# Performance work log

Hardware: AMD Instinct MI355X
Metric: run time of the kernel (lower is better)

## Reference

```python
import jax, jax.numpy as jnp
import numpy as np

NUM_HEADS = 4
NUM_GROUPS = 8
EPS = 1e-5


def setup_inputs() -> dict:
    key = jax.random.key(0)
    ks = jax.random.split(key, 5)
    B, C, H, W = 16, 512, 32, 32
    s = 1.0 / np.sqrt(C)
    return {
        "x": jax.random.normal(ks[0], (B, C, H, W), dtype=jnp.float32),
        "norm_w": jnp.ones((C,), jnp.float32),
        "norm_b": jnp.zeros((C,), jnp.float32),
        "q_w": jax.random.normal(ks[1], (C, C), jnp.float32) * s,
        "q_b": jnp.zeros((C,), jnp.float32),
        "k_w": jax.random.normal(ks[2], (C, C), jnp.float32) * s,
        "k_b": jnp.zeros((C,), jnp.float32),
        "v_w": jax.random.normal(ks[3], (C, C), jnp.float32) * s,
        "v_b": jnp.zeros((C,), jnp.float32),
        "p_w": jax.random.normal(ks[4], (C, C), jnp.float32) * s,
        "p_b": jnp.zeros((C,), jnp.float32),
    }


def _group_norm(x, w, b):
    # x: (B, C, N) -> GroupNorm over (C//G, N) per group
    B, C, N = x.shape
    g = x.reshape(B, NUM_GROUPS, C // NUM_GROUPS, N)
    mean = g.mean(axis=(2, 3), keepdims=True)
    var = g.var(axis=(2, 3), keepdims=True)
    g = (g - mean) * jax.lax.rsqrt(var + EPS)
    x = g.reshape(B, C, N)
    return x * w[None, :, None] + b[None, :, None]


def reference(x, norm_w, norm_b, q_w, q_b, k_w, k_b, v_w, v_b, p_w, p_b):
    B, C, H, W = x.shape
    N = H * W
    Ch = C // NUM_HEADS  # channels per head
    h = _group_norm(x.reshape(B, C, N), norm_w, norm_b)
    # 1x1 Conv1d == channel matmul: (o c, b c n -> b o n)
    q = jnp.einsum('oc,bcn->bon', q_w, h) + q_b[None, :, None]
    k = jnp.einsum('oc,bcn->bon', k_w, h) + k_b[None, :, None]
    v = jnp.einsum('oc,bcn->bon', v_w, h) + v_b[None, :, None]
    q = q.reshape(B, NUM_HEADS, Ch, N)
    k = k.reshape(B, NUM_HEADS, Ch, N)
    v = v.reshape(B, NUM_HEADS, Ch, N)
    attn = jnp.einsum('bhcn,bhcm->bhnm', q, k) * (1.0 / np.sqrt(Ch))
    attn = jax.nn.softmax(attn, axis=-1)
    out = jnp.einsum('bhnm,bhcm->bhcn', attn, v).reshape(B, C, N)
    out = jnp.einsum('oc,bcn->bon', p_w, out) + p_b[None, :, None]
    return x + out.reshape(B, C, H, W)
```

## Files before the change

kernel.cpp:

```cpp
#include <hip/hip_runtime.h>
#include <hip/hip_bf16.h>
#include <math.h>

#define B_    16
#define C_    512
#define N_    1024
#define G_    8
#define HEADS 4
#define CH    128
#define EPS   1e-5f

typedef __attribute__((ext_vector_type(8))) short short8;
typedef __attribute__((ext_vector_type(4))) float f32x4;
typedef __attribute__((ext_vector_type(16))) float f32x16;
typedef __attribute__((ext_vector_type(4))) int i32x4;

__device__ __forceinline__ unsigned short f2bf(float f) {
  union { float f; unsigned int i; } x; x.f = f;
  unsigned int r = x.i + 0x7FFFu + ((x.i >> 16) & 1u);
  return (unsigned short)(r >> 16);
}

__global__ __launch_bounds__(256) void gn_part(const float* __restrict__ x,
                                               float2* __restrict__ psum) {
  int blk = blockIdx.x;
  const float4* p4 = (const float4*)(x + (size_t)blk * 16384);
  float s = 0.f, ss = 0.f;
  for (int i = threadIdx.x; i < 4096; i += 256) {
    float4 v = p4[i];
    s  += v.x + v.y + v.z + v.w;
    ss += v.x * v.x + v.y * v.y + v.z * v.z + v.w * v.w;
  }
  for (int o = 32; o; o >>= 1) { s += __shfl_down(s, o); ss += __shfl_down(ss, o); }
  __shared__ float ls[4], lss[4];
  int wid = threadIdx.x >> 6, lane = threadIdx.x & 63;
  if (lane == 0) { ls[wid] = s; lss[wid] = ss; }
  __syncthreads();
  if (threadIdx.x == 0) {
    float2 r;
    r.x = (ls[0] + ls[1]) + (ls[2] + ls[3]);
    r.y = (lss[0] + lss[1]) + (lss[2] + lss[3]);
    psum[blk] = r;
  }
}

__global__ __launch_bounds__(256) void conv_w(const float* __restrict__ q, const float* __restrict__ k,
                                              const float* __restrict__ v, const float* __restrict__ p,
                                              const float* __restrict__ qb, const float* __restrict__ kb,
                                              unsigned short* __restrict__ dst,
                                              float* __restrict__ qkb) {
  const int n = C_ * C_;
  int i = blockIdx.x * 256 + threadIdx.x;
  if (i < n) {
    dst[i]         = f2bf(q[i]);
    dst[n + i]     = f2bf(k[i]);
    dst[2 * n + i] = f2bf(v[i]);
    dst[3 * n + i] = f2bf(p[i]);
  }
  if (i < 1024) qkb[i] = (i < 512) ? qb[i] : kb[i - 512];
}

__global__ __launch_bounds__(256) void gn_apply(const float* __restrict__ x,
                                                const float2* __restrict__ psum,
                                                const float* __restrict__ gw,
                                                const float* __restrict__ gb,
                                                unsigned short* __restrict__ hT) {
  __shared__ float T[64][65];
  int b = blockIdx.z, c0 = blockIdx.y * 64, n0 = blockIdx.x * 64;
  int bg = b * G_ + (c0 >> 6);
  float2 p0 = psum[bg * 4 + 0], p1 = psum[bg * 4 + 1];
  float2 p2 = psum[bg * 4 + 2], p3 = psum[bg * 4 + 3];
  const float inv = 1.f / ((C_ / G_) * N_);
  float mean = ((p0.x + p1.x) + (p2.x + p3.x)) * inv;
  float var  = ((p0.y + p1.y) + (p2.y + p3.y)) * inv - mean * mean;
  float rstd = rsqrtf(var + EPS);
  int t = threadIdx.x;
  for (int it = 0; it < 4; it++) {
    int L = it * 256 + t;
    int cc = L >> 4, nf = L & 15;
    float4 v = *(const float4*)&x[((size_t)b * C_ + c0 + cc) * N_ + n0 + nf * 4];
    float sw = gw[c0 + cc] * rstd, sb = gb[c0 + cc] - mean * sw;
    T[cc][nf * 4 + 0] = v.x * sw + sb;
    T[cc][nf * 4 + 1] = v.y * sw + sb;
    T[cc][nf * 4 + 2] = v.z * sw + sb;
    T[cc][nf * 4 + 3] = v.w * sw + sb;
  }
  __syncthreads();
  for (int it = 0; it < 4; it++) {
    int L = it * 256 + t;
    int nn = L >> 4, cv = L & 15;
    ushort4 o;
    o.x = f2bf(T[cv * 4 + 0][nn]);
    o.y = f2bf(T[cv * 4 + 1][nn]);
    o.z = f2bf(T[cv * 4 + 2][nn]);
    o.w = f2bf(T[cv * 4 + 3][nn]);
    *(ushort4*)&hT[((size_t)b * N_ + n0 + nn) * C_ + c0 + cv * 4] = o;
  }
}

template <bool OUT_BF16, bool BIAS_I, bool RESID>
__global__ __launch_bounds__(256) void gemm_tn(const unsigned short* __restrict__ A,
                                               const unsigned short* __restrict__ Bt,
                                               const float* __restrict__ bias,
                                               const float* __restrict__ resid,
                                               void* __restrict__ out,
                                               int Ncols, int K,
                                               long aBS, long bBS, long oBS) {
  __shared__ __align__(16) unsigned short As[128 * 64];
  __shared__ __align__(16) unsigned short Bs[128 * 64];
  const int lin = blockIdx.x;
  const int b = (lin & 7) * 2 + ((lin >> 3) & 1);
  const int rest = lin >> 4;
  const int bx = rest & 7, by = rest >> 3;
  const int i0 = by * 128, j0 = bx * 128;
  const unsigned short* Ab = A + (size_t)b * aBS + (size_t)i0 * K;
  const unsigned short* Bb = Bt + (size_t)b * bBS + (size_t)j0 * K;
  const int t = threadIdx.x, w = t >> 6, l = t & 63;
  const int wi = (w >> 1) * 64, wj = (w & 1) * 64;
  const int lr = l & 15, lk = (l >> 4) * 8;
  const int srow = l >> 3, scol = (l & 7) * 8;

  f32x4 acc[4][4];
  const f32x4 zf = {0.f, 0.f, 0.f, 0.f};
#pragma unroll
  for (int m = 0; m < 4; m++)
#pragma unroll
    for (int n = 0; n < 4; n++) acc[m][n] = zf;

  for (int kt = 0; kt < K; kt += 64) {
    __syncthreads();
#pragma unroll
    for (int i = 0; i < 4; i++) {
      int seg = w * 4 + i;
      int row = seg * 8 + srow;
      __builtin_amdgcn_global_load_lds(
          (const __attribute__((address_space(1))) void*)&Ab[(size_t)row * K + kt + scol],
          (__attribute__((address_space(3))) void*)&As[seg * 512], 16, 0, 0);
      __builtin_amdgcn_global_load_lds(
          (const __attribute__((address_space(1))) void*)&Bb[(size_t)row * K + kt + scol],
          (__attribute__((address_space(3))) void*)&Bs[seg * 512], 16, 0, 0);
    }
    __syncthreads();
#pragma unroll
    for (int ks = 0; ks < 64; ks += 32) {
      short8 af[4], bf[4];
#pragma unroll
      for (int m = 0; m < 4; m++) af[m] = *(const short8*)&As[(wi + m * 16 + lr) * 64 + ks + lk];
#pragma unroll
      for (int n = 0; n < 4; n++) bf[n] = *(const short8*)&Bs[(wj + n * 16 + lr) * 64 + ks + lk];
#pragma unroll
      for (int m = 0; m < 4; m++)
#pragma unroll
        for (int n = 0; n < 4; n++)
          acc[m][n] = __builtin_amdgcn_mfma_f32_16x16x32_bf16(af[m], bf[n], acc[m][n], 0, 0, 0);
    }
  }

  int rbase = (l >> 4) * 4;
#pragma unroll
  for (int m = 0; m < 4; m++) {
    int ig = i0 + wi + m * 16 + rbase;
#pragma unroll
    for (int n = 0; n < 4; n++) {
      int jg = j0 + wj + n * 16 + lr;
#pragma unroll
      for (int r = 0; r < 4; r++) {
        float vv = acc[m][n][r];
        vv += BIAS_I ? bias[ig + r] : bias[jg];
        size_t oidx = (size_t)b * oBS + (size_t)(ig + r) * Ncols + jg;
        if (RESID) vv += resid[oidx];
        if (OUT_BF16) ((unsigned short*)out)[oidx] = f2bf(vv);
        else ((float*)out)[oidx] = vv;
      }
    }
  }
}

__global__ __launch_bounds__(256, 2) void attn_kernel(const unsigned short* __restrict__ qkT,
                                                      const unsigned short* __restrict__ v,
                                                      unsigned short* __restrict__ aoT) {
  __shared__ __align__(16) unsigned short Ks[2][64 * 128];
  __shared__ __align__(16) unsigned short Vs[3][128 * 64];
  const int t = threadIdx.x, w = t >> 6, l = t & 63;
  const int h = l >> 5, l31 = l & 31, l7 = l & 7;
  const int lin = blockIdx.x;
  const int bh = (lin & 7) * 8 + ((lin >> 3) & 7);
  const int qt = lin >> 6;
  const int b = bh >> 2, hd = bh & 3, c0h = hd * CH;
  const int qg = qt * 128 + w * 32 + l31;
  const float sc2 = 0.08838834764831845f * 1.4426950408889634f;
  const float THRRAW = 11.5f / sc2;

  short8 qf[8];
  const unsigned short* qrow = qkT + ((size_t)b * N_ + qg) * 1024 + c0h;
#pragma unroll
  for (int kc = 0; kc < 8; kc++) qf[kc] = *(const short8*)&qrow[kc * 16 + h * 8];

  f32x16 o[4];
#pragma unroll
  for (int ct = 0; ct < 4; ct++) o[ct] = (f32x16)(0.f);
  float m = -INFINITY, lsum = 0.f;

  auto stageK = [&](int buf, int tt) {
    int mt = tt * 64;
#pragma unroll
    for (int i = 0; i < 4; i++) {
      int seg = w * 4 + i;
      int row = seg * 4 + (l >> 4);
      int gc = (l & 15) ^ (row & 7);
      const unsigned short* src = qkT + ((size_t)b * N_ + mt + row) * 1024 + 512 + c0h + gc * 8;
      __builtin_amdgcn_global_load_lds((const __attribute__((address_space(1))) void*)src,
                                       (__attribute__((address_space(3))) void*)&Ks[buf][seg * 512],
                                       16, 0, 0);
    }
  };
  auto stageV = [&](int buf, int tt) {
    int mt = tt * 64;
#pragma unroll
    for (int i = 0; i < 4; i++) {
      int seg = w * 4 + i;
      int row = seg * 8 + (l >> 3);
      int gc = (l & 7) ^ (row & 7);
      const unsigned short* src = v + ((size_t)b * C_ + c0h + row) * N_ + mt + gc * 8;
      __builtin_amdgcn_global_load_lds((const __attribute__((address_space(1))) void*)src,
                                       (__attribute__((address_space(3))) void*)&Vs[buf][seg * 512],
                                       16, 0, 0);
    }
  };

  stageK(0, 0); stageV(0, 0);
  stageK(1, 1); stageV(1, 1);
  __syncthreads();

  f32x16 st0 = (f32x16)(0.f), st1 = (f32x16)(0.f);
  {
    const unsigned short* KsB = &Ks[0][0];
#pragma unroll
    for (int kc = 0; kc < 8; kc++) {
      short8 kf0 = *(const short8*)&KsB[l31 * 128 + (((2 * kc + h) ^ l7) * 8)];
      short8 kf1 = *(const short8*)&KsB[(32 + l31) * 128 + (((2 * kc + h) ^ l7) * 8)];
      st0 = __builtin_amdgcn_mfma_f32_32x32x16_bf16(kf0, qf[kc], st0, 0, 0, 0);
      st1 = __builtin_amdgcn_mfma_f32_32x32x16_bf16(kf1, qf[kc], st1, 0, 0, 0);
    }
  }
  __syncthreads();

  for (int tt = 0; tt < 16; tt++) {
    if (tt < 14) { stageK(tt & 1, tt + 2); stageV((tt + 2) % 3, tt + 2); }

    float tr[16];
#pragma unroll
    for (int r = 0; r < 16; r++) tr[r] = fmaxf(st0[r], st1[r]);
#pragma unroll
    for (int s = 8; s >= 1; s >>= 1)
#pragma unroll
      for (int r = 0; r < s; r++) tr[r] = fmaxf(tr[r], tr[r + s]);
    float pmax = fmaxf(tr[0], __shfl_xor(tr[0], 32));

    bool skip = __all(pmax <= m + THRRAW);
    float mnew = skip ? m : fmaxf(m, pmax);
    float alpha = skip ? 1.f : exp2f((m - mnew) * sc2);
    float mb = mnew * sc2;
    m = mnew;

    float psg[4];
    short8 pf[4];
#pragma unroll
    for (int g = 0; g < 4; g++) {
      const int e0 = (g & 1) * 8;
      float p0, p1, p2, p3, p4, p5, p6, p7;
      if (g < 2) {
        p0 = exp2f(fmaf(st0[e0 + 0], sc2, -mb)); p1 = exp2f(fmaf(st0[e0 + 1], sc2, -mb));
        p2 = exp2f(fmaf(st0[e0 + 2], sc2, -mb)); p3 = exp2f(fmaf(st0[e0 + 3], sc2, -mb));
        p4 = exp2f(fmaf(st0[e0 + 4], sc2, -mb)); p5 = exp2f(fmaf(st0[e0 + 5], sc2, -mb));
        p6 = exp2f(fmaf(st0[e0 + 6], sc2, -mb)); p7 = exp2f(fmaf(st0[e0 + 7], sc2, -mb));
      } else {
        p0 = exp2f(fmaf(st1[e0 + 0], sc2, -mb)); p1 = exp2f(fmaf(st1[e0 + 1], sc2, -mb));
        p2 = exp2f(fmaf(st1[e0 + 2], sc2, -mb)); p3 = exp2f(fmaf(st1[e0 + 3], sc2, -mb));
        p4 = exp2f(fmaf(st1[e0 + 4], sc2, -mb)); p5 = exp2f(fmaf(st1[e0 + 5], sc2, -mb));
        p6 = exp2f(fmaf(st1[e0 + 6], sc2, -mb)); p7 = exp2f(fmaf(st1[e0 + 7], sc2, -mb));
      }
      psg[g] = ((p0 + p1) + (p2 + p3)) + ((p4 + p5) + (p6 + p7));
      unsigned int x, x2, y, y2;
      asm("v_cvt_pk_bf16_f32 %0, %1, %2" : "=v"(x)  : "v"(p0), "v"(p1));
      asm("v_cvt_pk_bf16_f32 %0, %1, %2" : "=v"(x2) : "v"(p2), "v"(p3));
      asm("v_cvt_pk_bf16_f32 %0, %1, %2" : "=v"(y)  : "v"(p4), "v"(p5));
      asm("v_cvt_pk_bf16_f32 %0, %1, %2" : "=v"(y2) : "v"(p6), "v"(p7));
      asm("v_permlane32_swap_b32 %0, %1" : "+v"(x), "+v"(y));
      asm("v_permlane32_swap_b32 %0, %1" : "+v"(x2), "+v"(y2));
      i32x4 pwv = {(int)x, (int)x2, (int)y, (int)y2};
      pf[g] = __builtin_bit_cast(short8, pwv);
    }
    float ps = (psg[0] + psg[1]) + (psg[2] + psg[3]);
    ps += __shfl_xor(ps, 32);
    lsum = lsum * alpha + ps;

    if (!skip) {
#pragma unroll
      for (int ct = 0; ct < 4; ct++)
#pragma unroll
        for (int r = 0; r < 16; r++) o[ct][r] *= alpha;
    }

    const unsigned short* VsB = &Vs[tt % 3][0];
    __builtin_amdgcn_s_setprio(1);
    if (tt < 15) {
      const unsigned short* KsN = &Ks[(tt + 1) & 1][0];
      f32x16 nst0 = (f32x16)(0.f), nst1 = (f32x16)(0.f);
#pragma unroll
      for (int kc = 0; kc < 8; kc++) {
        short8 kf0 = *(const short8*)&KsN[l31 * 128 + (((2 * kc + h) ^ l7) * 8)];
        short8 kf1 = *(const short8*)&KsN[(32 + l31) * 128 + (((2 * kc + h) ^ l7) * 8)];
        nst0 = __builtin_amdgcn_mfma_f32_32x32x16_bf16(kf0, qf[kc], nst0, 0, 0, 0);
        nst1 = __builtin_amdgcn_mfma_f32_32x32x16_bf16(kf1, qf[kc], nst1, 0, 0, 0);
        {
          int p = 2 * kc;
          int ct = p & 3, g = p >> 2;
          short8 vf = *(const short8*)&VsB[(ct * 32 + l31) * 64 + (((2 * g + h) ^ l7) * 8)];
          o[ct] = __builtin_amdgcn_mfma_f32_32x32x16_bf16(vf, pf[g], o[ct], 0, 0, 0);
          p = 2 * kc + 1;
          ct = p & 3; g = p >> 2;
          vf = *(const short8*)&VsB[(ct * 32 + l31) * 64 + (((2 * g + h) ^ l7) * 8)];
          o[ct] = __builtin_amdgcn_mfma_f32_32x32x16_bf16(vf, pf[g], o[ct], 0, 0, 0);
        }
      }
      __builtin_amdgcn_s_setprio(0);
      __syncthreads();
      st0 = nst0; st1 = nst1;
    } else {
#pragma unroll
      for (int p = 0; p < 16; p++) {
        int ct = p & 3, g = p >> 2;
        short8 vf = *(const short8*)&VsB[(ct * 32 + l31) * 64 + (((2 * g + h) ^ l7) * 8)];
        o[ct] = __builtin_amdgcn_mfma_f32_32x32x16_bf16(vf, pf[g], o[ct], 0, 0, 0);
      }
      __builtin_amdgcn_s_setprio(0);
    }
  }

  float rn = 1.f / lsum;
  unsigned short* orow = aoT + ((size_t)b * N_ + qg) * C_ + c0h;
#pragma unroll
  for (int ct = 0; ct < 4; ct++)
#pragma unroll
    for (int u = 0; u < 4; u++) {
      ushort4 ov;
      ov.x = f2bf(o[ct][u * 4 + 0] * rn);
      ov.y = f2bf(o[ct][u * 4 + 1] * rn);
      ov.z = f2bf(o[ct][u * 4 + 2] * rn);
      ov.w = f2bf(o[ct][u * 4 + 3] * rn);
      *(ushort4*)&orow[ct * 32 + u * 8 + h * 4] = ov;
    }
}

extern "C" void kernel_launch(void* const* d_in, const int* in_sizes, int n_in,
                              void* d_out, int out_size, void* d_ws, size_t ws_size,
                              hipStream_t stream) {
  const float* x  = (const float*)d_in[0];
  const float* nw = (const float*)d_in[1];
  const float* nb = (const float*)d_in[2];
  const float* qw = (const float*)d_in[3];
  const float* qb = (const float*)d_in[4];
  const float* kw = (const float*)d_in[5];
  const float* kb = (const float*)d_in[6];
  const float* vw = (const float*)d_in[7];
  const float* vb = (const float*)d_in[8];
  const float* pw = (const float*)d_in[9];
  const float* pb = (const float*)d_in[10];

  char* ws = (char*)d_ws;
  unsigned short* wbf  = (unsigned short*)ws;
  float2*         psum = (float2*)(ws + 0x200000);
  float*          qkb  = (float*)(ws + 0x201000);
  unsigned short* hT   = (unsigned short*)(ws + 0x202000);
  unsigned short* qkT  = (unsigned short*)(ws + 0x1202000);
  unsigned short* vv   = (unsigned short*)(ws + 0x3202000);
  unsigned short* aoT  = hT;

  const long NC = (long)N_ * C_;
  const int n_w = C_ * C_;

  gn_part<<<512, 256, 0, stream>>>(x, psum);
  conv_w<<<n_w / 256, 256, 0, stream>>>(qw, kw, vw, pw, qb, kb, wbf, qkb);
  gn_apply<<<dim3(N_ / 64, C_ / 64, B_), 256, 0, stream>>>(x, psum, nw, nb, hT);

  gemm_tn<true, false, false><<<dim3(1024), 256, 0, stream>>>(
      hT, wbf, qkb, nullptr, qkT, 1024, C_, NC, 0, (long)N_ * 1024);
  gemm_tn<true, true, false><<<dim3(512), 256, 0, stream>>>(
      wbf + 2 * n_w, hT, vb, nullptr, vv, N_, C_, 0, NC, NC);

  attn_kernel<<<dim3(512), 256, 0, stream>>>(qkT, vv, aoT);

  gemm_tn<false, true, true><<<dim3(512), 256, 0, stream>>>(
      wbf + 3 * n_w, aoT, pb, x, d_out, N_, C_, 0, NC, NC);
}
```

Before: 144.1 us.

## Load K fragments directly from global into registers instead of staging through LDS

Drops the LDS double buffer for K in the attention kernel. Each lane now loads its own K fragments straight from global memory into registers, one tile ahead, while V is still staged through LDS. V source pointers are precomputed and advanced each step. This removes the LDS writes and reads for K and frees shared memory, but it adds 16 short8 registers per lane and every wave now issues its own redundant global K loads, which raises register pressure and L2 traffic.

```diff
diff --git a/kernel.cpp b/kernel.cpp
--- a/kernel.cpp
+++ b/kernel.cpp
@@ -179,7 +179,6 @@
 __global__ __launch_bounds__(256, 2) void attn_kernel(const unsigned short* __restrict__ qkT,
                                                       const unsigned short* __restrict__ v,
                                                       unsigned short* __restrict__ aoT) {
-  __shared__ __align__(16) unsigned short Ks[2][64 * 128];
   __shared__ __align__(16) unsigned short Vs[3][128 * 64];
   const int t = threadIdx.x, w = t >> 6, l = t & 63;
   const int h = l >> 5, l31 = l & 31, l7 = l & 7;
@@ -201,52 +200,53 @@
   for (int ct = 0; ct < 4; ct++) o[ct] = (f32x16)(0.f);
   float m = -INFINITY, lsum = 0.f;
 
-  auto stageK = [&](int buf, int tt) {
-    int mt = tt * 64;
+  const unsigned short* kp0 = qkT + ((size_t)b * N_ + l31) * 1024 + 512 + c0h + h * 8;
+  const unsigned short* kp1 = kp0 + (size_t)32 * 1024;
+  short8 ka[8], kb[8];
+  auto loadK = [&]() {
+#pragma unroll
+    for (int kc = 0; kc < 8; kc++) {
+      ka[kc] = *(const short8*)(kp0 + kc * 16);
+      kb[kc] = *(const short8*)(kp1 + kc * 16);
+    }
+    kp0 += (size_t)64 * 1024;
+    kp1 += (size_t)64 * 1024;
+  };
+
+  const unsigned short* vsrc[4];
+#pragma unroll
+  for (int i = 0; i < 4; i++) {
+    int seg = w * 4 + i;
+    int row = seg * 8 + (l >> 3);
+    int gc = (l & 7) ^ (row & 7);
+    vsrc[i] = v + ((size_t)b * C_ + c0h + row) * N_ + gc * 8;
+  }
+  auto stageV = [&](int buf) {
+    unsigned short* VsD = &Vs[buf][0];
 #pragma unroll
     for (int i = 0; i < 4; i++) {
       int seg = w * 4 + i;
-      int row = seg * 4 + (l >> 4);
-      int gc = (l & 15) ^ (row & 7);
-      const unsigned short* src = qkT + ((size_t)b * N_ + mt + row) * 1024 + 512 + c0h + gc * 8;
-      __builtin_amdgcn_global_load_lds((const __attribute__((address_space(1))) void*)src,
-                                       (__attribute__((address_space(3))) void*)&Ks[buf][seg * 512],
+      __builtin_amdgcn_global_load_lds((const __attribute__((address_space(1))) void*)vsrc[i],
+                                       (__attribute__((address_space(3))) void*)&VsD[seg * 512],
                                        16, 0, 0);
+      vsrc[i] += 64;
     }
   };
-  auto stageV = [&](int buf, int tt) {
-    int mt = tt * 64;
-#pragma unroll
-    for (int i = 0; i < 4; i++) {
-      int seg = w * 4 + i;
-      int row = seg * 8 + (l >> 3);
-      int gc = (l & 7) ^ (row & 7);
-      const unsigned short* src = v + ((size_t)b * C_ + c0h + row) * N_ + mt + gc * 8;
-      __builtin_amdgcn_global_load_lds((const __attribute__((address_space(1))) void*)src,
-                                       (__attribute__((address_space(3))) void*)&Vs[buf][seg * 512],
-                                       16, 0, 0);
-    }
-  };
-
-  stageK(0, 0); stageV(0, 0);
-  stageK(1, 1); stageV(1, 1);
+
+  stageV(0);
+  stageV(1);
+  loadK();
+  f32x16 st0 = (f32x16)(0.f), st1 = (f32x16)(0.f);
+#pragma unroll
+  for (int kc = 0; kc < 8; kc++) {
+    st0 = __builtin_amdgcn_mfma_f32_32x32x16_bf16(ka[kc], qf[kc], st0, 0, 0, 0);
+    st1 = __builtin_amdgcn_mfma_f32_32x32x16_bf16(kb[kc], qf[kc], st1, 0, 0, 0);
+  }
   __syncthreads();
 
-  f32x16 st0 = (f32x16)(0.f), st1 = (f32x16)(0.f);
-  {
-    const unsigned short* KsB = &Ks[0][0];
-#pragma unroll
-    for (int kc = 0; kc < 8; kc++) {
-      short8 kf0 = *(const short8*)&KsB[l31 * 128 + (((2 * kc + h) ^ l7) * 8)];
-      short8 kf1 = *(const short8*)&KsB[(32 + l31) * 128 + (((2 * kc + h) ^ l7) * 8)];
-      st0 = __builtin_amdgcn_mfma_f32_32x32x16_bf16(kf0, qf[kc], st0, 0, 0, 0);
-      st1 = __builtin_amdgcn_mfma_f32_32x32x16_bf16(kf1, qf[kc], st1, 0, 0, 0);
-    }
-  }
-  __syncthreads();
-
   for (int tt = 0; tt < 16; tt++) {
-    if (tt < 14) { stageK(tt & 1, tt + 2); stageV((tt + 2) % 3, tt + 2); }
+    if (tt < 15) loadK();
+    if (tt < 14) stageV((tt + 2) % 3);
 
     float tr[16];
 #pragma unroll
@@ -305,14 +305,11 @@
     const unsigned short* VsB = &Vs[tt % 3][0];
     __builtin_amdgcn_s_setprio(1);
     if (tt < 15) {
-      const unsigned short* KsN = &Ks[(tt + 1) & 1][0];
       f32x16 nst0 = (f32x16)(0.f), nst1 = (f32x16)(0.f);
 #pragma unroll
       for (int kc = 0; kc < 8; kc++) {
-        short8 kf0 = *(const short8*)&KsN[l31 * 128 + (((2 * kc + h) ^ l7) * 8)];
-        short8 kf1 = *(const short8*)&KsN[(32 + l31) * 128 + (((2 * kc + h) ^ l7) * 8)];
-        nst0 = __builtin_amdgcn_mfma_f32_32x32x16_bf16(kf0, qf[kc], nst0, 0, 0, 0);
-        nst1 = __builtin_amdgcn_mfma_f32_32x32x16_bf16(kf1, qf[kc], nst1, 0, 0, 0);
+        nst0 = __builtin_amdgcn_mfma_f32_32x32x16_bf16(ka[kc], qf[kc], nst0, 0, 0, 0);
+        nst1 = __builtin_amdgcn_mfma_f32_32x32x16_bf16(kb[kc], qf[kc], nst1, 0, 0, 0);
         {
           int p = 2 * kc;
           int ct = p & 3, g = p >> 2;
```

New measurement: 167.6 us. +16.3%, slower.

## Reschedule attention loop to overlap next QK^T MFMAs with softmax

Applied to the files above, without the earlier changes.

Restructures the flash-attention main loop so the next tile's QK^T MFMAs are issued in two halves around the max-reduction softmax step, instead of interleaving them with the PV MFMAs after softmax. The last iteration is peeled into a separate block, and the s_setprio calls are removed. Global-to-LDS source addresses are precomputed once and advanced by pointer increments, and the cross-half shuffles are replaced with v_permlane32_swap. The aim is to hide exp/max VALU latency behind matrix work and to cut address arithmetic, at the cost of more live registers and some duplicated code.

```diff
diff --git a/kernel.cpp b/kernel.cpp
--- a/kernel.cpp
+++ b/kernel.cpp
@@ -201,35 +201,35 @@
   for (int ct = 0; ct < 4; ct++) o[ct] = (f32x16)(0.f);
   float m = -INFINITY, lsum = 0.f;
 
-  auto stageK = [&](int buf, int tt) {
-    int mt = tt * 64;
+  const unsigned short* ksrcp[4];
+  const unsigned short* vsrcp[4];
+#pragma unroll
+  for (int i = 0; i < 4; i++) {
+    int seg = w * 4 + i;
+    int rowK = seg * 4 + (l >> 4);
+    int gcK = (l & 15) ^ (rowK & 7);
+    ksrcp[i] = qkT + ((size_t)b * N_ + rowK) * 1024 + 512 + c0h + gcK * 8;
+    int rowV = seg * 8 + (l >> 3);
+    int gcV = (l & 7) ^ (rowV & 7);
+    vsrcp[i] = v + ((size_t)b * C_ + c0h + rowV) * N_ + gcV * 8;
+  }
+  auto stage = [&](int kbuf, int vbuf) {
 #pragma unroll
     for (int i = 0; i < 4; i++) {
       int seg = w * 4 + i;
-      int row = seg * 4 + (l >> 4);
-      int gc = (l & 15) ^ (row & 7);
-      const unsigned short* src = qkT + ((size_t)b * N_ + mt + row) * 1024 + 512 + c0h + gc * 8;
-      __builtin_amdgcn_global_load_lds((const __attribute__((address_space(1))) void*)src,
-                                       (__attribute__((address_space(3))) void*)&Ks[buf][seg * 512],
+      __builtin_amdgcn_global_load_lds((const __attribute__((address_space(1))) void*)ksrcp[i],
+                                       (__attribute__((address_space(3))) void*)&Ks[kbuf][seg * 512],
                                        16, 0, 0);
+      ksrcp[i] += (size_t)64 * 1024;
+      __builtin_amdgcn_global_load_lds((const __attribute__((address_space(1))) void*)vsrcp[i],
+                                       (__attribute__((address_space(3))) void*)&Vs[vbuf][seg * 512],
+                                       16, 0, 0);
+      vsrcp[i] += 64;
     }
   };
-  auto stageV = [&](int buf, int tt) {
-    int mt = tt * 64;
-#pragma unroll
-    for (int i = 0; i < 4; i++) {
-      int seg = w * 4 + i;
-      int row = seg * 8 + (l >> 3);
-      int gc = (l & 7) ^ (row & 7);
-      const unsigned short* src = v + ((size_t)b * C_ + c0h + row) * N_ + mt + gc * 8;
-      __builtin_amdgcn_global_load_lds((const __attribute__((address_space(1))) void*)src,
-                                       (__attribute__((address_space(3))) void*)&Vs[buf][seg * 512],
-                                       16, 0, 0);
-    }
-  };
-
-  stageK(0, 0); stageV(0, 0);
-  stageK(1, 1); stageV(1, 1);
+
+  stage(0, 0);
+  stage(1, 1);
   __syncthreads();
 
   f32x16 st0 = (f32x16)(0.f), st1 = (f32x16)(0.f);
@@ -245,8 +245,20 @@
   }
   __syncthreads();
 
-  for (int tt = 0; tt < 16; tt++) {
-    if (tt < 14) { stageK(tt & 1, tt + 2); stageV((tt + 2) % 3, tt + 2); }
+  for (int tt = 0; tt < 15; tt++) {
+    if (tt < 14) stage(tt & 1, (tt + 2) % 3);
+
+    const unsigned short* KsN = &Ks[(tt + 1) & 1][0];
+    const unsigned short* VsB = &Vs[tt % 3][0];
+    f32x16 nst0 = (f32x16)(0.f), nst1 = (f32x16)(0.f);
+
+#pragma unroll
+    for (int kc = 0; kc < 4; kc++) {
+      short8 kf0 = *(const short8*)&KsN[l31 * 128 + (((2 * kc + h) ^ l7) * 8)];
+      short8 kf1 = *(const short8*)&KsN[(32 + l31) * 128 + (((2 * kc + h) ^ l7) * 8)];
+      nst0 = __builtin_amdgcn_mfma_f32_32x32x16_bf16(kf0, qf[kc], nst0, 0, 0, 0);
+      nst1 = __builtin_amdgcn_mfma_f32_32x32x16_bf16(kf1, qf[kc], nst1, 0, 0, 0);
+    }
 
     float tr[16];
 #pragma unroll
@@ -255,13 +267,23 @@
     for (int s = 8; s >= 1; s >>= 1)
 #pragma unroll
       for (int r = 0; r < s; r++) tr[r] = fmaxf(tr[r], tr[r + s]);
-    float pmax = fmaxf(tr[0], __shfl_xor(tr[0], 32));
+    float px0 = tr[0], px1 = tr[0];
+    asm volatile("v_permlane32_swap_b32 %0, %1" : "+v"(px0), "+v"(px1));
+    float pmax = fmaxf(px0, px1);
 
     bool skip = __all(pmax <= m + THRRAW);
     float mnew = skip ? m : fmaxf(m, pmax);
     float alpha = skip ? 1.f : exp2f((m - mnew) * sc2);
     float mb = mnew * sc2;
     m = mnew;
+
+#pragma unroll
+    for (int kc = 4; kc < 8; kc++) {
+      short8 kf0 = *(const short8*)&KsN[l31 * 128 + (((2 * kc + h) ^ l7) * 8)];
+      short8 kf1 = *(const short8*)&KsN[(32 + l31) * 128 + (((2 * kc + h) ^ l7) * 8)];
+      nst0 = __builtin_amdgcn_mfma_f32_32x32x16_bf16(kf0, qf[kc], nst0, 0, 0, 0);
+      nst1 = __builtin_amdgcn_mfma_f32_32x32x16_bf16(kf1, qf[kc], nst1, 0, 0, 0);
+    }
 
     float psg[4];
     short8 pf[4];
@@ -292,7 +314,9 @@
       pf[g] = __builtin_bit_cast(short8, pwv);
     }
     float ps = (psg[0] + psg[1]) + (psg[2] + psg[3]);
-    ps += __shfl_xor(ps, 32);
+    float s0 = ps, s1 = ps;
+    asm volatile("v_permlane32_swap_b32 %0, %1" : "+v"(s0), "+v"(s1));
+    ps = s0 + s1;
     lsum = lsum * alpha + ps;
 
     if (!skip) {
@@ -302,39 +326,82 @@
         for (int r = 0; r < 16; r++) o[ct][r] *= alpha;
     }
 
-    const unsigned short* VsB = &Vs[tt % 3][0];
-    __builtin_amdgcn_s_setprio(1);
-    if (tt < 15) {
-      const unsigned short* KsN = &Ks[(tt + 1) & 1][0];
-      f32x16 nst0 = (f32x16)(0.f), nst1 = (f32x16)(0.f);
-#pragma unroll
-      for (int kc = 0; kc < 8; kc++) {
-        short8 kf0 = *(const short8*)&KsN[l31 * 128 + (((2 * kc + h) ^ l7) * 8)];
-        short8 kf1 = *(const short8*)&KsN[(32 + l31) * 128 + (((2 * kc + h) ^ l7) * 8)];
-        nst0 = __builtin_amdgcn_mfma_f32_32x32x16_bf16(kf0, qf[kc], nst0, 0, 0, 0);
-        nst1 = __builtin_amdgcn_mfma_f32_32x32x16_bf16(kf1, qf[kc], nst1, 0, 0, 0);
-        {
-          int p = 2 * kc;
-          int ct = p & 3, g = p >> 2;
-          short8 vf = *(const short8*)&VsB[(ct * 32 + l31) * 64 + (((2 * g + h) ^ l7) * 8)];
-          o[ct] = __builtin_amdgcn_mfma_f32_32x32x16_bf16(vf, pf[g], o[ct], 0, 0, 0);
-          p = 2 * kc + 1;
-          ct = p & 3; g = p >> 2;
-          vf = *(const short8*)&VsB[(ct * 32 + l31) * 64 + (((2 * g + h) ^ l7) * 8)];
-          o[ct] = __builtin_amdgcn_mfma_f32_32x32x16_bf16(vf, pf[g], o[ct], 0, 0, 0);
-        }
+#pragma unroll
+    for (int p = 0; p < 16; p++) {
+      int ct = p & 3, g = p >> 2;
+      short8 vf = *(const short8*)&VsB[(ct * 32 + l31) * 64 + (((2 * g + h) ^ l7) * 8)];
+      o[ct] = __builtin_amdgcn_mfma_f32_32x32x16_bf16(vf, pf[g], o[ct], 0, 0, 0);
+    }
+
+    __syncthreads();
+    st0 = nst0; st1 = nst1;
+  }
+
+  {
+    const unsigned short* VsB = &Vs[15 % 3][0];
+    float tr[16];
+#pragma unroll
+    for (int r = 0; r < 16; r++) tr[r] = fmaxf(st0[r], st1[r]);
+#pragma unroll
+    for (int s = 8; s >= 1; s >>= 1)
+#pragma unroll
+      for (int r = 0; r < s; r++) tr[r] = fmaxf(tr[r], tr[r + s]);
+    float px0 = tr[0], px1 = tr[0];
+    asm volatile("v_permlane32_swap_b32 %0, %1" : "+v"(px0), "+v"(px1));
+    float pmax = fmaxf(px0, px1);
+
+    bool skip = __all(pmax <= m + THRRAW);
+    float mnew = skip ? m : fmaxf(m, pmax);
+    float alpha = skip ? 1.f : exp2f((m - mnew) * sc2);
+    float mb = mnew * sc2;
+    m = mnew;
+
+    float psg[4];
+    short8 pf[4];
+#pragma unroll
+    for (int g = 0; g < 4; g++) {
+      const int e0 = (g & 1) * 8;
+      float p0, p1, p2, p3, p4, p5, p6, p7;
+      if (g < 2) {
+        p0 = exp2f(fmaf(st0[e0 + 0], sc2, -mb)); p1 = exp2f(fmaf(st0[e0 + 1], sc2, -mb));
+        p2 = exp2f(fmaf(st0[e0 + 2], sc2, -mb)); p3 = exp2f(fmaf(st0[e0 + 3], sc2, -mb));
+        p4 = exp2f(fmaf(st0[e0 + 4], sc2, -mb)); p5 = exp2f(fmaf(st0[e0 + 5], sc2, -mb));
+        p6 = exp2f(fmaf(st0[e0 + 6], sc2, -mb)); p7 = exp2f(fmaf(st0[e0 + 7], sc2, -mb));
+      } else {
+        p0 = exp2f(fmaf(st1[e0 + 0], sc2, -mb)); p1 = exp2f(fmaf(st1[e0 + 1], sc2, -mb));
+        p2 = exp2f(fmaf(st1[e0 + 2], sc2, -mb)); p3 = exp2f(fmaf(st1[e0 + 3], sc2, -mb));
+        p4 = exp2f(fmaf(st1[e0 + 4], sc2, -mb)); p5 = exp2f(fmaf(st1[e0 + 5], sc2, -mb));
+        p6 = exp2f(fmaf(st1[e0 + 6], sc2, -mb)); p7 = exp2f(fmaf(st1[e0 + 7], sc2, -mb));
       }
-      __builtin_amdgcn_s_setprio(0);
-      __syncthreads();
-      st0 = nst0; st1 = nst1;
-    } else {
-#pragma unroll
-      for (int p = 0; p < 16; p++) {
-        int ct = p & 3, g = p >> 2;
-        short8 vf = *(const short8*)&VsB[(ct * 32 + l31) * 64 + (((2 * g + h) ^ l7) * 8)];
-        o[ct] = __builtin_amdgcn_mfma_f32_32x32x16_bf16(vf, pf[g], o[ct], 0, 0, 0);
-      }
-      __builtin_amdgcn_s_setprio(0);
+      psg[g] = ((p0 + p1) + (p2 + p3)) + ((p4 + p5) + (p6 + p7));
+      unsigned int x, x2, y, y2;
+      asm("v_cvt_pk_bf16_f32 %0, %1, %2" : "=v"(x)  : "v"(p0), "v"(p1));
+      asm("v_cvt_pk_bf16_f32 %0, %1, %2" : "=v"(x2) : "v"(p2), "v"(p3));
+      asm("v_cvt_pk_bf16_f32 %0, %1, %2" : "=v"(y)  : "v"(p4), "v"(p5));
+      asm("v_cvt_pk_bf16_f32 %0, %1, %2" : "=v"(y2) : "v"(p6), "v"(p7));
+      asm("v_permlane32_swap_b32 %0, %1" : "+v"(x), "+v"(y));
+      asm("v_permlane32_swap_b32 %0, %1" : "+v"(x2), "+v"(y2));
+      i32x4 pwv = {(int)x, (int)x2, (int)y, (int)y2};
+      pf[g] = __builtin_bit_cast(short8, pwv);
+    }
+    float ps = (psg[0] + psg[1]) + (psg[2] + psg[3]);
+    float s0 = ps, s1 = ps;
+    asm volatile("v_permlane32_swap_b32 %0, %1" : "+v"(s0), "+v"(s1));
+    ps = s0 + s1;
+    lsum = lsum * alpha + ps;
+
+    if (!skip) {
+#pragma unroll
+      for (int ct = 0; ct < 4; ct++)
+#pragma unroll
+        for (int r = 0; r < 16; r++) o[ct][r] *= alpha;
+    }
+
+#pragma unroll
+    for (int p = 0; p < 16; p++) {
+      int ct = p & 3, g = p >> 2;
+      short8 vf = *(const short8*)&VsB[(ct * 32 + l31) * 64 + (((2 * g + h) ^ l7) * 8)];
+      o[ct] = __builtin_amdgcn_mfma_f32_32x32x16_bf16(vf, pf[g], o[ct], 0, 0, 0);
     }
   }
 
```

Measured after the change: 143.8 us. No clear change (-0.2%).
